# Optimization experiments

Hardware: AMD Instinct MI355X
Metric: run time of the kernel (lower is better)

Reference implementation:

```python
import jax, jax.numpy as jnp
import numpy as np

ALPHA = 0.5
SMOOTH = 1e-05
ITERS = 10


def _max_pool3x3(x):
    # 3x3 max pool, stride 1, SAME padding on NCHW tensor
    return jax.lax.reduce_window(
        x, -jnp.inf, jax.lax.max,
        window_dimensions=(1, 1, 3, 3),
        window_strides=(1, 1, 1, 1),
        padding='SAME')


def _soft_erode(x):
    return -_max_pool3x3(-x)


def _soft_dilate(x):
    return _max_pool3x3(x)


def _soft_skeletonize(img, iterations=ITERS):
    def body(skel, _):
        eroded = _soft_erode(skel)
        temp = _soft_dilate(eroded)
        skel = skel - (skel - eroded) * temp
        skel = jnp.clip(skel, 0.0, 1.0)
        return skel, None
    skel, _ = jax.lax.scan(body, img, None, length=iterations)
    return skel


def _dice_score(pred, target, smooth=SMOOTH):
    inter = jnp.sum(pred * target, axis=(2, 3))
    union = jnp.sum(pred, axis=(2, 3)) + jnp.sum(target, axis=(2, 3))
    dice = (2.0 * inter + smooth) / (union + smooth)
    return jnp.mean(dice)


def setup_inputs() -> dict:
    key = jax.random.key(0)
    k1, k2 = jax.random.split(key)
    B, C, H, W = 32, 1, 512, 512
    pred_logits = jax.random.normal(k1, (B, C, H, W), dtype=jnp.float32)
    target = jax.random.uniform(k2, (B, C, H, W), dtype=jnp.float32)
    return {"pred_logits": pred_logits, "target": target}


def reference(pred_logits, target):
    pred = jax.nn.sigmoid(pred_logits)
    dice = _dice_score(pred, target)
    pred_skel = _soft_skeletonize(pred)
    target_skel = _soft_skeletonize(target)
    skel_dice = _dice_score(pred_skel, target_skel)
    loss = (1.0 - ALPHA) * (1.0 - dice) + ALPHA * (1.0 - skel_dice)
    return (loss, dice, skel_dice)
```

## Files before the change

### kernel.cpp

```cpp
#include <hip/hip_runtime.h>
#include <hip/hip_fp16.h>
#include <math.h>


#define H 512
#define W 512
#define IMG (H * W)
#define NIMG 64
#define NPRED 32

#define APU 40
#define AROWS 74
#define BP2 38
#define BROWS 68

#define PINF2 0x7C007C00u
#define NINF2 0xFC00FC00u
#define ONE2  0x3C003C00u

typedef _Float16 f16;
typedef _Float16 h2 __attribute__((ext_vector_type(2)));
typedef __fp16 fp16v2 __attribute__((ext_vector_type(2)));

__device__ __forceinline__ uint pack2(float a, float b) {
    fp16v2 h = __builtin_amdgcn_cvt_pkrtz(a, b);
    return __builtin_bit_cast(uint, h);
}

__device__ __forceinline__ uint pmin(uint a, uint b) {
    uint d; asm("v_pk_min_f16 %0, %1, %2" : "=v"(d) : "v"(a), "v"(b)); return d;
}
__device__ __forceinline__ uint pmax(uint a, uint b) {
    uint d; asm("v_pk_max_f16 %0, %1, %2" : "=v"(d) : "v"(a), "v"(b)); return d;
}
__device__ __forceinline__ uint abit(uint hi, uint lo) {
    return __builtin_amdgcn_alignbit(hi, lo, 16);
}

__device__ __forceinline__ float wsum64(float v) {
#pragma unroll
    for (int o = 32; o > 0; o >>= 1) v += __shfl_down(v, o);
    return v;
}

__device__ __forceinline__ void hmin4p(const uint* __restrict__ p, uint m[4], uint sc[2]) {
    uint2 w0 = *(const uint2*)(p);
    uint2 w1 = *(const uint2*)(p + 2);
    uint2 w2 = *(const uint2*)(p + 4);
    sc[0] = w1.x; sc[1] = w1.y;
    uint s01 = abit(w0.y, w0.x);
    uint s12 = abit(w1.x, w0.y);
    uint s23 = abit(w1.y, w1.x);
    uint s34 = abit(w2.x, w1.y);
    uint s45 = abit(w2.y, w2.x);
    m[0] = pmin(s01, pmin(w0.y, s12));
    m[1] = pmin(s12, pmin(w1.x, s23));
    m[2] = pmin(s23, pmin(w1.y, s34));
    m[3] = pmin(s34, pmin(w2.x, s45));
}

__device__ __forceinline__ void erodep(const uint a[4], const uint b[4], const uint c[4],
                                       bool rowok, const bool eok[4], uint e[4]) {
#pragma unroll
    for (int i = 0; i < 4; i++) {
        uint v = pmin(a[i], pmin(b[i], c[i]));
        e[i] = (rowok && eok[i]) ? v : NINF2;
    }
}

__device__ __forceinline__ void hmaxp(const uint e[4], uint hx[2], uint ec[2]) {
    uint a12 = abit(e[1], e[0]);
    uint a23 = abit(e[2], e[1]);
    uint a34 = abit(e[3], e[2]);
    hx[0] = pmax(a12, pmax(e[1], a23));
    hx[1] = pmax(a23, pmax(e[2], a34));
    ec[0] = e[1]; ec[1] = e[2];
}

__device__ __forceinline__ uint upd_pair(uint s, uint ec, uint t) {
    h2 sh = __builtin_bit_cast(h2, s);
    h2 eh = __builtin_bit_cast(h2, ec);
    h2 th = __builtin_bit_cast(h2, t);
    h2 o = sh - (sh - eh) * th;
    return pmin(pmax(__builtin_bit_cast(uint, o), 0u), ONE2);
}

template<int SIG>
__device__ float2 fillA_f32p(uint* __restrict__ A, const float* __restrict__ src,
                             const float* __restrict__ tgt,
                             int tileX, int tileY, int tid) {
    float a = 0.0f, b = 0.0f;
    for (int it = tid; it < AROWS * 20; it += 256) {
        int r = it / 20;
        int u2 = it - r * 20;
        int gy = tileY + r - 4;
        int gx = tileX - 8 + 4 * u2;
        uint2 v = make_uint2(PINF2, PINF2);
        if (r < 72 && (unsigned)(u2 - 1) < 18u && (unsigned)gy < (unsigned)H &&
            (unsigned)gx < (unsigned)W) {
            float4 f = *(const float4*)(src + (size_t)gy * W + gx);
            if (SIG) {
                f.x = 1.0f / (1.0f + __expf(-f.x));
                f.y = 1.0f / (1.0f + __expf(-f.y));
                f.z = 1.0f / (1.0f + __expf(-f.z));
                f.w = 1.0f / (1.0f + __expf(-f.w));
            }
            if (((unsigned)(gx - tileX) < 64u) && ((unsigned)(gy - tileY) < 64u)) {
                if (SIG) {
                    float4 t = *(const float4*)(tgt + (size_t)gy * W + gx);
                    a += f.x * t.x + f.y * t.y + f.z * t.z + f.w * t.w;
                    b += f.x + f.y + f.z + f.w;
                } else {
                    a += f.x + f.y + f.z + f.w;
                }
            }
            v.x = pack2(f.x, f.y);
            v.y = pack2(f.z, f.w);
        }
        *(uint2*)(A + r * APU + 2 * u2) = v;
    }
    return make_float2(a, b);
}

__device__ void fillA_f16p(uint* __restrict__ A, const f16* __restrict__ src,
                           int tileX, int tileY, int tid) {
    for (int it = tid; it < AROWS * 20; it += 256) {
        int r = it / 20;
        int u2 = it - r * 20;
        int gy = tileY + r - 4;
        int gx = tileX - 8 + 4 * u2;
        uint2 v = make_uint2(PINF2, PINF2);
        if (r < 72 && (unsigned)(u2 - 1) < 18u && (unsigned)gy < (unsigned)H &&
            (unsigned)gx < (unsigned)W) {
            v = *(const uint2*)(src + (size_t)gy * W + gx);
        }
        *(uint2*)(A + r * APU + 2 * u2) = v;
    }
}

__device__ void stage1(const uint* __restrict__ Au, uint* __restrict__ Bu,
                       int tileX, int tileY, int tid) {
    for (int item = tid; item < 252; item += 256) {
        const int s = item / 18;
        const int q = item - s * 18;
        const int gcb = tileX - 4 + 4 * q;
        const int ys = tileY - 2 + 5 * s;
        bool eok[4], wok[2];
#pragma unroll
        for (int i = 0; i < 4; i++) eok[i] = ((unsigned)(gcb - 2 + 2 * i) < 511u);
        wok[0] = ((unsigned)gcb < 511u);
        wok[1] = ((unsigned)(gcb + 2) < 511u);
        const int lr = 5 * s + 2;
        const uint* Ab = Au + 2 * q;
        uint m[3][4], sc[3][2], hx[3][2], e[4], ec_cur[2], ec_nxt[2], tsc[2];
        hmin4p(Ab + (lr - 2) * APU, m[0], tsc);
        hmin4p(Ab + (lr - 1) * APU, m[1], tsc);
        hmin4p(Ab + (lr + 0) * APU, m[2], sc[0]);
        erodep(m[0], m[1], m[2], (unsigned)(ys - 1) < (unsigned)H, eok, e);
        hmaxp(e, hx[0], ec_nxt);
        hmin4p(Ab + (lr + 1) * APU, m[0], sc[1]);
        erodep(m[1], m[2], m[0], (unsigned)ys < (unsigned)H, eok, e);
        hmaxp(e, hx[1], ec_cur);
#pragma unroll
        for (int k = 0; k < 5; k++) {
            hmin4p(Ab + (lr + 2 + k) * APU, m[(k + 1) % 3], sc[(2 + k) % 3]);
            erodep(m[(k + 2) % 3], m[k % 3], m[(k + 1) % 3],
                   (unsigned)(ys + k + 1) < (unsigned)H, eok, e);
            hmaxp(e, hx[(k + 2) % 3], ec_nxt);
            int br = 5 * s + k;
            if (br < BROWS) {
                uint t0 = pmax(hx[k % 3][0], pmax(hx[(k + 1) % 3][0], hx[(k + 2) % 3][0]));
                uint t1 = pmax(hx[k % 3][1], pmax(hx[(k + 1) % 3][1], hx[(k + 2) % 3][1]));
                uint o0 = upd_pair(sc[k % 3][0], ec_cur[0], t0);
                uint o1 = upd_pair(sc[k % 3][1], ec_cur[1], t1);
                bool rin = ((unsigned)(ys + k) < (unsigned)H);
                uint2 wv;
                wv.x = (rin && wok[0]) ? o0 : PINF2;
                wv.y = (rin && wok[1]) ? o1 : PINF2;
                *(uint2*)(Bu + br * BP2 + 2 * q) = wv;
            }
            ec_cur[0] = ec_nxt[0]; ec_cur[1] = ec_nxt[1];
        }
    }
}

template<bool TOREG>
__device__ void stage2(const uint* __restrict__ Bu, int tileX, int tileY,
                       int tx, int ty, f16* __restrict__ gdst, float (*oreg)[4]) {
    const int X = tileX + 4 * tx;
    const int gy0 = tileY + 4 * ty;
    const int rb = 4 * ty + 2;
    bool eok[4];
    eok[0] = (X != 0);
    eok[1] = true;
    eok[2] = true;
    eok[3] = (X + 4 < W);
    const uint* Bb = Bu + 2 * tx;
    uint m[3][4], sc[3][2], hx[3][2], e[4], ec_cur[2], ec_nxt[2], tsc[2];
    hmin4p(Bb + (rb - 2) * BP2, m[0], tsc);
    hmin4p(Bb + (rb - 1) * BP2, m[1], tsc);
    hmin4p(Bb + (rb + 0) * BP2, m[2], sc[0]);
    erodep(m[0], m[1], m[2], (unsigned)(gy0 - 1) < (unsigned)H, eok, e);
    hmaxp(e, hx[0], ec_nxt);
    hmin4p(Bb + (rb + 1) * BP2, m[0], sc[1]);
    erodep(m[1], m[2], m[0], true, eok, e);
    hmaxp(e, hx[1], ec_cur);
#pragma unroll
    for (int k = 0; k < 4; k++) {
        hmin4p(Bb + (rb + 2 + k) * BP2, m[(k + 1) % 3], sc[(2 + k) % 3]);
        erodep(m[(k + 2) % 3], m[k % 3], m[(k + 1) % 3],
               (unsigned)(gy0 + k + 1) < (unsigned)H, eok, e);
        hmaxp(e, hx[(k + 2) % 3], ec_nxt);
        uint t0 = pmax(hx[k % 3][0], pmax(hx[(k + 1) % 3][0], hx[(k + 2) % 3][0]));
        uint t1 = pmax(hx[k % 3][1], pmax(hx[(k + 1) % 3][1], hx[(k + 2) % 3][1]));
        uint o0 = upd_pair(sc[k % 3][0], ec_cur[0], t0);
        uint o1 = upd_pair(sc[k % 3][1], ec_cur[1], t1);
        if (TOREG) {
            h2 a = __builtin_bit_cast(h2, o0);
            h2 b = __builtin_bit_cast(h2, o1);
            oreg[k][0] = (float)a.x; oreg[k][1] = (float)a.y;
            oreg[k][2] = (float)b.x; oreg[k][3] = (float)b.y;
        } else {
            *(uint2*)(gdst + (size_t)(gy0 + k) * W + X) = make_uint2(o0, o1);
        }
        ec_cur[0] = ec_nxt[0]; ec_cur[1] = ec_nxt[1];
    }
}

__global__ __launch_bounds__(256, 6) void k_first(
    const float* __restrict__ logits, const float* __restrict__ target,
    f16* __restrict__ outb, float* __restrict__ parts0, float* __restrict__ parts1) {
    __shared__ __align__(16) uint A[AROWS * APU];
    __shared__ __align__(16) uint Bu[BROWS * BP2];
    __shared__ float red[8];
    const int img = blockIdx.z;
    const int tileX = blockIdx.x * 64, tileY = blockIdx.y * 64;
    const int tid = threadIdx.y * 16 + threadIdx.x;
    const bool pred = (img < NPRED);
    float2 ab;
    if (pred) ab = fillA_f32p<1>(A, logits + (size_t)img * IMG,
                                 target + (size_t)img * IMG, tileX, tileY, tid);
    else      ab = fillA_f32p<0>(A, target + (size_t)(img - NPRED) * IMG,
                                 nullptr, tileX, tileY, tid);
    __syncthreads();
    float a = wsum64(ab.x), b = wsum64(ab.y);
    if ((tid & 63) == 0) { red[tid >> 6] = a; red[4 + (tid >> 6)] = b; }
    stage1(A, Bu, tileX, tileY, tid);
    __syncthreads();
    if (tid == 0) {
        int bi = blockIdx.z * 64 + blockIdx.y * 8 + blockIdx.x;
        parts0[bi] = red[0] + red[1] + red[2] + red[3];
        parts1[bi] = red[4] + red[5] + red[6] + red[7];
    }
    stage2<false>(Bu, tileX, tileY, threadIdx.x, threadIdx.y,
                  outb + (size_t)img * IMG, nullptr);
}

__global__ __launch_bounds__(256, 6) void k_mid(
    const f16* __restrict__ in, f16* __restrict__ outb) {
    __shared__ __align__(16) uint A[AROWS * APU];
    __shared__ __align__(16) uint Bu[BROWS * BP2];
    const int img = blockIdx.z;
    const int tileX = blockIdx.x * 64, tileY = blockIdx.y * 64;
    const int tid = threadIdx.y * 16 + threadIdx.x;
    fillA_f16p(A, in + (size_t)img * IMG, tileX, tileY, tid);
    __syncthreads();
    stage1(A, Bu, tileX, tileY, tid);
    __syncthreads();
    stage2<false>(Bu, tileX, tileY, threadIdx.x, threadIdx.y,
                  outb + (size_t)img * IMG, nullptr);
}

__global__ __launch_bounds__(256, 6) void k_last(
    const f16* __restrict__ in, float* __restrict__ pA,
    float* __restrict__ pB, float* __restrict__ pC) {
    __shared__ __align__(16) uint A[AROWS * APU];
    __shared__ __align__(16) uint Bu[BROWS * BP2];
    __shared__ float red[12];
    const int img = blockIdx.z;
    const int tileX = blockIdx.x * 64, tileY = blockIdx.y * 64;
    const int tid = threadIdx.y * 16 + threadIdx.x;
    float op[4][4], ot[4][4];
    fillA_f16p(A, in + (size_t)img * IMG, tileX, tileY, tid);
    __syncthreads();
    stage1(A, Bu, tileX, tileY, tid);
    __syncthreads();
    stage2<true>(Bu, tileX, tileY, threadIdx.x, threadIdx.y, nullptr, op);
    fillA_f16p(A, in + (size_t)(img + NPRED) * IMG, tileX, tileY, tid);
    __syncthreads();
    stage1(A, Bu, tileX, tileY, tid);
    __syncthreads();
    stage2<true>(Bu, tileX, tileY, threadIdx.x, threadIdx.y, nullptr, ot);
    float a = 0.0f, b = 0.0f, c = 0.0f;
#pragma unroll
    for (int k = 0; k < 4; k++)
#pragma unroll
        for (int j = 0; j < 4; j++) {
            a += op[k][j] * ot[k][j];
            b += op[k][j];
            c += ot[k][j];
        }
    a = wsum64(a); b = wsum64(b); c = wsum64(c);
    if ((tid & 63) == 0) {
        red[tid >> 6] = a; red[4 + (tid >> 6)] = b; red[8 + (tid >> 6)] = c;
    }
    __syncthreads();
    if (tid == 0) {
        int bi = img * 64 + blockIdx.y * 8 + blockIdx.x;
        pA[bi] = red[0] + red[1] + red[2] + red[3];
        pB[bi] = red[4] + red[5] + red[6] + red[7];
        pC[bi] = red[8] + red[9] + red[10] + red[11];
    }
}

__global__ __launch_bounds__(64) void finalize_img(
    const float* __restrict__ parts0, const float* __restrict__ parts1,
    const float* __restrict__ pA, const float* __restrict__ pB,
    const float* __restrict__ pC, float* __restrict__ dices) {
    const int i = blockIdx.x, t = threadIdx.x;
    float inter = wsum64(parts0[i * 64 + t]);
    float sp = wsum64(parts1[i * 64 + t]);
    float st = wsum64(parts0[(NPRED + i) * 64 + t]);
    float i2 = wsum64(pA[i * 64 + t]);
    float sp2 = wsum64(pB[i * 64 + t]);
    float st2 = wsum64(pC[i * 64 + t]);
    if (t == 0) {
        dices[i] = (float)((2.0 * (double)inter + 1e-5) / ((double)sp + (double)st + 1e-5));
        dices[32 + i] = (float)((2.0 * (double)i2 + 1e-5) / ((double)sp2 + (double)st2 + 1e-5));
    }
}

__global__ void finalize_out(const float* __restrict__ dices, float* __restrict__ out) {
    const int t = threadIdx.x;
    double d = 0.0, sd = 0.0;
    if (t < 32) { d = dices[t]; sd = dices[32 + t]; }
#pragma unroll
    for (int o = 32; o > 0; o >>= 1) { d += __shfl_down(d, o); sd += __shfl_down(sd, o); }
    if (t == 0) {
        d *= (1.0 / 32.0); sd *= (1.0 / 32.0);
        out[0] = (float)(0.5 * (1.0 - d) + 0.5 * (1.0 - sd));
        out[1] = (float)d;
        out[2] = (float)sd;
    }
}

extern "C" void kernel_launch(void* const* d_in, const int* in_sizes, int n_in,
                              void* d_out, int out_size, void* d_ws, size_t ws_size,
                              hipStream_t stream) {
    (void)in_sizes; (void)n_in; (void)out_size; (void)ws_size;
    const float* logits = (const float*)d_in[0];
    const float* target = (const float*)d_in[1];
    float* out = (float*)d_out;
    f16* buf0 = (f16*)d_ws;
    f16* buf1 = buf0 + (size_t)NIMG * IMG;
    float* parts0 = (float*)(buf1 + (size_t)NIMG * IMG);
    float* parts1 = parts0 + 4096;
    float* pA = parts1 + 4096;
    float* pB = pA + 2048;
    float* pC = pB + 2048;
    float* dices = pC + 2048;

    dim3 blk(16, 16, 1);
    k_first<<<dim3(8, 8, NIMG), blk, 0, stream>>>(logits, target, buf0, parts0, parts1);
    k_mid<<<dim3(8, 8, NIMG), blk, 0, stream>>>(buf0, buf1);
    k_mid<<<dim3(8, 8, NIMG), blk, 0, stream>>>(buf1, buf0);
    k_mid<<<dim3(8, 8, NIMG), blk, 0, stream>>>(buf0, buf1);
    k_last<<<dim3(8, 8, NPRED), blk, 0, stream>>>(buf1, pA, pB, pC);
    finalize_img<<<32, 64, 0, stream>>>(parts0, parts1, pA, pB, pC, dices);
    finalize_out<<<1, 64, 0, stream>>>(dices, out);
}
```

Baseline: 265.6 us.

## Widen tiles to 128x64 with 8-pixel-per-thread work and edge-specialized interior paths

Tiles grow from 64x64 to 128x64, and each thread now handles 8 fp16 pixels per row using 16-byte LDS and global accesses instead of 4. This shrinks the relative halo overhead, both in redundant loads and in recomputed halo rows and columns. Kernels are templated on an EDGE flag so interior blocks skip all boundary predicates. The trade-offs are more registers per thread (launch bounds lowered from 6 to 4 blocks), fewer blocks overall, and larger LDS tiles.

```diff
diff --git a/kernel.cpp b/kernel.cpp
--- a/kernel.cpp
+++ b/kernel.cpp
@@ -9,10 +9,13 @@
 #define NIMG 64
 #define NPRED 32
 
-#define APU 40
+#define APU 72
 #define AROWS 74
-#define BP2 38
+#define BPU 68
 #define BROWS 68
+#define TQ 17
+#define S1ITEMS 238
+#define FILLN (AROWS * 18)
 
 #define PINF2 0x7C007C00u
 #define NINF2 0xFC00FC00u
@@ -22,11 +25,14 @@
 typedef _Float16 h2 __attribute__((ext_vector_type(2)));
 typedef __fp16 fp16v2 __attribute__((ext_vector_type(2)));
 
+__device__ __forceinline__ float2 unpack2(uint u) {
+    fp16v2 h = __builtin_bit_cast(fp16v2, u);
+    return make_float2((float)h.x, (float)h.y);
+}
 __device__ __forceinline__ uint pack2(float a, float b) {
     fp16v2 h = __builtin_amdgcn_cvt_pkrtz(a, b);
     return __builtin_bit_cast(uint, h);
 }
-
 __device__ __forceinline__ uint pmin(uint a, uint b) {
     uint d; asm("v_pk_min_f16 %0, %1, %2" : "=v"(d) : "v"(a), "v"(b)); return d;
 }
@@ -43,38 +49,37 @@
     return v;
 }
 
-__device__ __forceinline__ void hmin4p(const uint* __restrict__ p, uint m[4], uint sc[2]) {
-    uint2 w0 = *(const uint2*)(p);
-    uint2 w1 = *(const uint2*)(p + 2);
-    uint2 w2 = *(const uint2*)(p + 4);
-    sc[0] = w1.x; sc[1] = w1.y;
-    uint s01 = abit(w0.y, w0.x);
-    uint s12 = abit(w1.x, w0.y);
-    uint s23 = abit(w1.y, w1.x);
-    uint s34 = abit(w2.x, w1.y);
-    uint s45 = abit(w2.y, w2.x);
-    m[0] = pmin(s01, pmin(w0.y, s12));
-    m[1] = pmin(s12, pmin(w1.x, s23));
-    m[2] = pmin(s23, pmin(w1.y, s34));
-    m[3] = pmin(s34, pmin(w2.x, s45));
-}
-
-__device__ __forceinline__ void erodep(const uint a[4], const uint b[4], const uint c[4],
-                                       bool rowok, const bool eok[4], uint e[4]) {
-#pragma unroll
-    for (int i = 0; i < 4; i++) {
+__device__ __forceinline__ void hmin8p(const uint* __restrict__ p, uint m[6], uint sc[4]) {
+    uint4 w0 = *(const uint4*)(p);
+    uint4 w1 = *(const uint4*)(p + 4);
+    uint w[8] = {w0.x, w0.y, w0.z, w0.w, w1.x, w1.y, w1.z, w1.w};
+    sc[0] = w[2]; sc[1] = w[3]; sc[2] = w[4]; sc[3] = w[5];
+    uint s[7];
+#pragma unroll
+    for (int j = 0; j < 7; j++) s[j] = abit(w[j + 1], w[j]);
+#pragma unroll
+    for (int i = 0; i < 6; i++) m[i] = pmin(s[i], pmin(w[i + 1], s[i + 1]));
+}
+
+template<bool EDGE>
+__device__ __forceinline__ void erode8(const uint a[6], const uint b[6], const uint c[6],
+                                       bool rowok, const bool* eok, uint e[6]) {
+#pragma unroll
+    for (int i = 0; i < 6; i++) {
         uint v = pmin(a[i], pmin(b[i], c[i]));
-        e[i] = (rowok && eok[i]) ? v : NINF2;
-    }
-}
-
-__device__ __forceinline__ void hmaxp(const uint e[4], uint hx[2], uint ec[2]) {
-    uint a12 = abit(e[1], e[0]);
-    uint a23 = abit(e[2], e[1]);
-    uint a34 = abit(e[3], e[2]);
-    hx[0] = pmax(a12, pmax(e[1], a23));
-    hx[1] = pmax(a23, pmax(e[2], a34));
-    ec[0] = e[1]; ec[1] = e[2];
+        e[i] = EDGE ? ((rowok && eok[i]) ? v : NINF2) : v;
+    }
+}
+
+__device__ __forceinline__ void hmax8(const uint e[6], uint hx[4], uint ec[4]) {
+    uint a[5];
+#pragma unroll
+    for (int j = 0; j < 5; j++) a[j] = abit(e[j + 1], e[j]);
+#pragma unroll
+    for (int p = 0; p < 4; p++) {
+        hx[p] = pmax(a[p], pmax(e[p + 1], a[p + 1]));
+        ec[p] = e[p + 1];
+    }
 }
 
 __device__ __forceinline__ uint upd_pair(uint s, uint ec, uint t) {
@@ -85,228 +90,284 @@
     return pmin(pmax(__builtin_bit_cast(uint, o), 0u), ONE2);
 }
 
-template<int SIG>
-__device__ float2 fillA_f32p(uint* __restrict__ A, const float* __restrict__ src,
-                             const float* __restrict__ tgt,
-                             int tileX, int tileY, int tid) {
+template<bool EDGE, int SIG>
+__device__ float2 fillA_f32(uint* __restrict__ A, const float* __restrict__ src,
+                            const float* __restrict__ tgt,
+                            int tileX, int tileY, int tid) {
     float a = 0.0f, b = 0.0f;
-    for (int it = tid; it < AROWS * 20; it += 256) {
-        int r = it / 20;
-        int u2 = it - r * 20;
-        int gy = tileY + r - 4;
-        int gx = tileX - 8 + 4 * u2;
-        uint2 v = make_uint2(PINF2, PINF2);
-        if (r < 72 && (unsigned)(u2 - 1) < 18u && (unsigned)gy < (unsigned)H &&
-            (unsigned)gx < (unsigned)W) {
-            float4 f = *(const float4*)(src + (size_t)gy * W + gx);
+    for (int i = tid; i < FILLN; i += 256) {
+        const int r = i / 18;
+        const int q = i - 18 * r;
+        const int gy = tileY + r - 4;
+        const int gx = tileX - 8 + 8 * q;
+        uint4 v = make_uint4(PINF2, PINF2, PINF2, PINF2);
+        const bool ok = EDGE ? (r < 72 && (unsigned)gy < (unsigned)H &&
+                                (unsigned)gx < (unsigned)W)
+                             : true;
+        if (ok) {
+            const float* sp = src + (size_t)gy * W + gx;
+            float4 f0 = *(const float4*)(sp);
+            float4 f1 = *(const float4*)(sp + 4);
             if (SIG) {
-                f.x = 1.0f / (1.0f + __expf(-f.x));
-                f.y = 1.0f / (1.0f + __expf(-f.y));
-                f.z = 1.0f / (1.0f + __expf(-f.z));
-                f.w = 1.0f / (1.0f + __expf(-f.w));
+                f0.x = 1.0f / (1.0f + __expf(-f0.x));
+                f0.y = 1.0f / (1.0f + __expf(-f0.y));
+                f0.z = 1.0f / (1.0f + __expf(-f0.z));
+                f0.w = 1.0f / (1.0f + __expf(-f0.w));
+                f1.x = 1.0f / (1.0f + __expf(-f1.x));
+                f1.y = 1.0f / (1.0f + __expf(-f1.y));
+                f1.z = 1.0f / (1.0f + __expf(-f1.z));
+                f1.w = 1.0f / (1.0f + __expf(-f1.w));
             }
-            if (((unsigned)(gx - tileX) < 64u) && ((unsigned)(gy - tileY) < 64u)) {
+            if (((unsigned)(r - 4) < 64u) && ((unsigned)(q - 1) < 16u)) {
                 if (SIG) {
-                    float4 t = *(const float4*)(tgt + (size_t)gy * W + gx);
-                    a += f.x * t.x + f.y * t.y + f.z * t.z + f.w * t.w;
-                    b += f.x + f.y + f.z + f.w;
+                    const float* tp = tgt + (size_t)gy * W + gx;
+                    float4 t0 = *(const float4*)(tp);
+                    float4 t1 = *(const float4*)(tp + 4);
+                    a += f0.x * t0.x + f0.y * t0.y + f0.z * t0.z + f0.w * t0.w
+                       + f1.x * t1.x + f1.y * t1.y + f1.z * t1.z + f1.w * t1.w;
+                    b += f0.x + f0.y + f0.z + f0.w + f1.x + f1.y + f1.z + f1.w;
                 } else {
-                    a += f.x + f.y + f.z + f.w;
+                    a += f0.x + f0.y + f0.z + f0.w + f1.x + f1.y + f1.z + f1.w;
                 }
             }
-            v.x = pack2(f.x, f.y);
-            v.y = pack2(f.z, f.w);
+            v.x = pack2(f0.x, f0.y); v.y = pack2(f0.z, f0.w);
+            v.z = pack2(f1.x, f1.y); v.w = pack2(f1.z, f1.w);
         }
-        *(uint2*)(A + r * APU + 2 * u2) = v;
+        *(uint4*)(A + r * APU + 4 * q) = v;
     }
     return make_float2(a, b);
 }
 
-__device__ void fillA_f16p(uint* __restrict__ A, const f16* __restrict__ src,
-                           int tileX, int tileY, int tid) {
-    for (int it = tid; it < AROWS * 20; it += 256) {
-        int r = it / 20;
-        int u2 = it - r * 20;
-        int gy = tileY + r - 4;
-        int gx = tileX - 8 + 4 * u2;
-        uint2 v = make_uint2(PINF2, PINF2);
-        if (r < 72 && (unsigned)(u2 - 1) < 18u && (unsigned)gy < (unsigned)H &&
-            (unsigned)gx < (unsigned)W) {
-            v = *(const uint2*)(src + (size_t)gy * W + gx);
+template<bool EDGE>
+__device__ void fillA_f16(uint* __restrict__ A, const f16* __restrict__ src,
+                          int tileX, int tileY, int tid) {
+    for (int i = tid; i < FILLN; i += 256) {
+        const int r = i / 18;
+        const int q = i - 18 * r;
+        const int gy = tileY + r - 4;
+        const int gx = tileX - 8 + 8 * q;
+        uint4 v;
+        if (EDGE) {
+            v = make_uint4(PINF2, PINF2, PINF2, PINF2);
+            if (r < 72 && (unsigned)gy < (unsigned)H && (unsigned)gx < (unsigned)W)
+                v = *(const uint4*)(src + (size_t)gy * W + gx);
+        } else {
+            v = *(const uint4*)(src + (size_t)gy * W + gx);
         }
-        *(uint2*)(A + r * APU + 2 * u2) = v;
-    }
-}
-
+        *(uint4*)(A + r * APU + 4 * q) = v;
+    }
+}
+
+template<bool EDGE>
 __device__ void stage1(const uint* __restrict__ Au, uint* __restrict__ Bu,
                        int tileX, int tileY, int tid) {
-    for (int item = tid; item < 252; item += 256) {
-        const int s = item / 18;
-        const int q = item - s * 18;
-        const int gcb = tileX - 4 + 4 * q;
-        const int ys = tileY - 2 + 5 * s;
-        bool eok[4], wok[2];
-#pragma unroll
-        for (int i = 0; i < 4; i++) eok[i] = ((unsigned)(gcb - 2 + 2 * i) < 511u);
-        wok[0] = ((unsigned)gcb < 511u);
-        wok[1] = ((unsigned)(gcb + 2) < 511u);
-        const int lr = 5 * s + 2;
-        const uint* Ab = Au + 2 * q;
-        uint m[3][4], sc[3][2], hx[3][2], e[4], ec_cur[2], ec_nxt[2], tsc[2];
-        hmin4p(Ab + (lr - 2) * APU, m[0], tsc);
-        hmin4p(Ab + (lr - 1) * APU, m[1], tsc);
-        hmin4p(Ab + (lr + 0) * APU, m[2], sc[0]);
-        erodep(m[0], m[1], m[2], (unsigned)(ys - 1) < (unsigned)H, eok, e);
-        hmaxp(e, hx[0], ec_nxt);
-        hmin4p(Ab + (lr + 1) * APU, m[0], sc[1]);
-        erodep(m[1], m[2], m[0], (unsigned)ys < (unsigned)H, eok, e);
-        hmaxp(e, hx[1], ec_cur);
-#pragma unroll
-        for (int k = 0; k < 5; k++) {
-            hmin4p(Ab + (lr + 2 + k) * APU, m[(k + 1) % 3], sc[(2 + k) % 3]);
-            erodep(m[(k + 2) % 3], m[k % 3], m[(k + 1) % 3],
-                   (unsigned)(ys + k + 1) < (unsigned)H, eok, e);
-            hmaxp(e, hx[(k + 2) % 3], ec_nxt);
-            int br = 5 * s + k;
-            if (br < BROWS) {
-                uint t0 = pmax(hx[k % 3][0], pmax(hx[(k + 1) % 3][0], hx[(k + 2) % 3][0]));
-                uint t1 = pmax(hx[k % 3][1], pmax(hx[(k + 1) % 3][1], hx[(k + 2) % 3][1]));
-                uint o0 = upd_pair(sc[k % 3][0], ec_cur[0], t0);
-                uint o1 = upd_pair(sc[k % 3][1], ec_cur[1], t1);
-                bool rin = ((unsigned)(ys + k) < (unsigned)H);
-                uint2 wv;
-                wv.x = (rin && wok[0]) ? o0 : PINF2;
-                wv.y = (rin && wok[1]) ? o1 : PINF2;
-                *(uint2*)(Bu + br * BP2 + 2 * q) = wv;
+    if (tid >= S1ITEMS) return;
+    const int s = tid / TQ;
+    const int g = tid - TQ * s;
+    const int gcb = tileX + 8 * g - 4;
+    const int ys = tileY - 2 + 5 * s;
+    bool eok[6], wok[4];
+    if (EDGE) {
+#pragma unroll
+        for (int i = 0; i < 6; i++) eok[i] = ((unsigned)(gcb - 2 + 2 * i) < (unsigned)W);
+#pragma unroll
+        for (int p = 0; p < 4; p++) wok[p] = ((unsigned)(gcb + 2 * p) < (unsigned)W);
+    }
+    const int lr = 5 * s + 2;
+    const uint* Ab = Au + 4 * g;
+    uint m[3][6], sc[3][4], hx[3][4], e[6], ec_cur[4], ec_nxt[4], tsc[4];
+    hmin8p(Ab + (lr - 2) * APU, m[0], tsc);
+    hmin8p(Ab + (lr - 1) * APU, m[1], tsc);
+    hmin8p(Ab + (lr + 0) * APU, m[2], sc[0]);
+    erode8<EDGE>(m[0], m[1], m[2], (unsigned)(ys - 1) < (unsigned)H, eok, e);
+    hmax8(e, hx[0], ec_nxt);
+    hmin8p(Ab + (lr + 1) * APU, m[0], sc[1]);
+    erode8<EDGE>(m[1], m[2], m[0], (unsigned)ys < (unsigned)H, eok, e);
+    hmax8(e, hx[1], ec_cur);
+#pragma unroll
+    for (int k = 0; k < 5; k++) {
+        hmin8p(Ab + (lr + 2 + k) * APU, m[(k + 1) % 3], sc[(2 + k) % 3]);
+        erode8<EDGE>(m[(k + 2) % 3], m[k % 3], m[(k + 1) % 3],
+                     (unsigned)(ys + k + 1) < (unsigned)H, eok, e);
+        hmax8(e, hx[(k + 2) % 3], ec_nxt);
+        const int br = 5 * s + k;
+        if (br < BROWS) {
+            const bool rin = EDGE ? ((unsigned)(ys + k) < (unsigned)H) : true;
+            uint o[4];
+#pragma unroll
+            for (int p = 0; p < 4; p++) {
+                uint t = pmax(hx[k % 3][p], pmax(hx[(k + 1) % 3][p], hx[(k + 2) % 3][p]));
+                uint v = upd_pair(sc[k % 3][p], ec_cur[p], t);
+                o[p] = EDGE ? ((rin && wok[p]) ? v : PINF2) : v;
             }
-            ec_cur[0] = ec_nxt[0]; ec_cur[1] = ec_nxt[1];
+            *(uint4*)(Bu + br * BPU + 4 * g) = make_uint4(o[0], o[1], o[2], o[3]);
         }
-    }
-}
-
-template<bool TOREG>
-__device__ void stage2(const uint* __restrict__ Bu, int tileX, int tileY,
-                       int tx, int ty, f16* __restrict__ gdst, float (*oreg)[4]) {
-    const int X = tileX + 4 * tx;
+#pragma unroll
+        for (int p = 0; p < 4; p++) ec_cur[p] = ec_nxt[p];
+    }
+}
+
+template<bool EDGE, bool TOREG>
+__device__ void stage2(const uint* __restrict__ Bu, int tileX, int tileY, int tid,
+                       f16* __restrict__ gdst, uint* __restrict__ oreg) {
+    const int g = tid & 15;
+    const int ty = tid >> 4;
+    const int X = tileX + 8 * g;
     const int gy0 = tileY + 4 * ty;
     const int rb = 4 * ty + 2;
-    bool eok[4];
-    eok[0] = (X != 0);
-    eok[1] = true;
-    eok[2] = true;
-    eok[3] = (X + 4 < W);
-    const uint* Bb = Bu + 2 * tx;
-    uint m[3][4], sc[3][2], hx[3][2], e[4], ec_cur[2], ec_nxt[2], tsc[2];
-    hmin4p(Bb + (rb - 2) * BP2, m[0], tsc);
-    hmin4p(Bb + (rb - 1) * BP2, m[1], tsc);
-    hmin4p(Bb + (rb + 0) * BP2, m[2], sc[0]);
-    erodep(m[0], m[1], m[2], (unsigned)(gy0 - 1) < (unsigned)H, eok, e);
-    hmaxp(e, hx[0], ec_nxt);
-    hmin4p(Bb + (rb + 1) * BP2, m[0], sc[1]);
-    erodep(m[1], m[2], m[0], true, eok, e);
-    hmaxp(e, hx[1], ec_cur);
+    bool eok[6];
+    if (EDGE) {
+#pragma unroll
+        for (int i = 0; i < 6; i++) eok[i] = ((unsigned)(X - 2 + 2 * i) < (unsigned)W);
+    }
+    const uint* Bb = Bu + 4 * g;
+    uint m[3][6], sc[3][4], hx[3][4], e[6], ec_cur[4], ec_nxt[4], tsc[4];
+    hmin8p(Bb + (rb - 2) * BPU, m[0], tsc);
+    hmin8p(Bb + (rb - 1) * BPU, m[1], tsc);
+    hmin8p(Bb + (rb + 0) * BPU, m[2], sc[0]);
+    erode8<EDGE>(m[0], m[1], m[2], (unsigned)(gy0 - 1) < (unsigned)H, eok, e);
+    hmax8(e, hx[0], ec_nxt);
+    hmin8p(Bb + (rb + 1) * BPU, m[0], sc[1]);
+    erode8<EDGE>(m[1], m[2], m[0], true, eok, e);
+    hmax8(e, hx[1], ec_cur);
 #pragma unroll
     for (int k = 0; k < 4; k++) {
-        hmin4p(Bb + (rb + 2 + k) * BP2, m[(k + 1) % 3], sc[(2 + k) % 3]);
-        erodep(m[(k + 2) % 3], m[k % 3], m[(k + 1) % 3],
-               (unsigned)(gy0 + k + 1) < (unsigned)H, eok, e);
-        hmaxp(e, hx[(k + 2) % 3], ec_nxt);
-        uint t0 = pmax(hx[k % 3][0], pmax(hx[(k + 1) % 3][0], hx[(k + 2) % 3][0]));
-        uint t1 = pmax(hx[k % 3][1], pmax(hx[(k + 1) % 3][1], hx[(k + 2) % 3][1]));
-        uint o0 = upd_pair(sc[k % 3][0], ec_cur[0], t0);
-        uint o1 = upd_pair(sc[k % 3][1], ec_cur[1], t1);
+        hmin8p(Bb + (rb + 2 + k) * BPU, m[(k + 1) % 3], sc[(2 + k) % 3]);
+        erode8<EDGE>(m[(k + 2) % 3], m[k % 3], m[(k + 1) % 3],
+                     (unsigned)(gy0 + k + 1) < (unsigned)H, eok, e);
+        hmax8(e, hx[(k + 2) % 3], ec_nxt);
+        uint o[4];
+#pragma unroll
+        for (int p = 0; p < 4; p++) {
+            uint t = pmax(hx[k % 3][p], pmax(hx[(k + 1) % 3][p], hx[(k + 2) % 3][p]));
+            o[p] = upd_pair(sc[k % 3][p], ec_cur[p], t);
+        }
         if (TOREG) {
-            h2 a = __builtin_bit_cast(h2, o0);
-            h2 b = __builtin_bit_cast(h2, o1);
-            oreg[k][0] = (float)a.x; oreg[k][1] = (float)a.y;
-            oreg[k][2] = (float)b.x; oreg[k][3] = (float)b.y;
+#pragma unroll
+            for (int p = 0; p < 4; p++) oreg[4 * k + p] = o[p];
         } else {
-            *(uint2*)(gdst + (size_t)(gy0 + k) * W + X) = make_uint2(o0, o1);
+            *(uint4*)(gdst + (size_t)(gy0 + k) * W + X) = make_uint4(o[0], o[1], o[2], o[3]);
         }
-        ec_cur[0] = ec_nxt[0]; ec_cur[1] = ec_nxt[1];
-    }
-}
-
-__global__ __launch_bounds__(256, 6) void k_first(
+#pragma unroll
+        for (int p = 0; p < 4; p++) ec_cur[p] = ec_nxt[p];
+    }
+}
+
+__device__ __forceinline__ bool is_edge() {
+    return (blockIdx.x == 0) | (blockIdx.x == 3) | (blockIdx.y == 0) | (blockIdx.y == 7);
+}
+
+__global__ __launch_bounds__(256, 4) void k_first(
     const float* __restrict__ logits, const float* __restrict__ target,
     f16* __restrict__ outb, float* __restrict__ parts0, float* __restrict__ parts1) {
     __shared__ __align__(16) uint A[AROWS * APU];
-    __shared__ __align__(16) uint Bu[BROWS * BP2];
+    __shared__ __align__(16) uint Bu[BROWS * BPU];
     __shared__ float red[8];
     const int img = blockIdx.z;
-    const int tileX = blockIdx.x * 64, tileY = blockIdx.y * 64;
-    const int tid = threadIdx.y * 16 + threadIdx.x;
+    const int tileX = blockIdx.x * 128, tileY = blockIdx.y * 64;
+    const int tid = threadIdx.x;
     const bool pred = (img < NPRED);
+    const bool edge = is_edge();
     float2 ab;
-    if (pred) ab = fillA_f32p<1>(A, logits + (size_t)img * IMG,
-                                 target + (size_t)img * IMG, tileX, tileY, tid);
-    else      ab = fillA_f32p<0>(A, target + (size_t)(img - NPRED) * IMG,
-                                 nullptr, tileX, tileY, tid);
+    if (edge) {
+        if (pred) ab = fillA_f32<true, 1>(A, logits + (size_t)img * IMG,
+                                          target + (size_t)img * IMG, tileX, tileY, tid);
+        else      ab = fillA_f32<true, 0>(A, target + (size_t)(img - NPRED) * IMG,
+                                          nullptr, tileX, tileY, tid);
+    } else {
+        if (pred) ab = fillA_f32<false, 1>(A, logits + (size_t)img * IMG,
+                                           target + (size_t)img * IMG, tileX, tileY, tid);
+        else      ab = fillA_f32<false, 0>(A, target + (size_t)(img - NPRED) * IMG,
+                                           nullptr, tileX, tileY, tid);
+    }
     __syncthreads();
     float a = wsum64(ab.x), b = wsum64(ab.y);
     if ((tid & 63) == 0) { red[tid >> 6] = a; red[4 + (tid >> 6)] = b; }
-    stage1(A, Bu, tileX, tileY, tid);
+    if (edge) stage1<true>(A, Bu, tileX, tileY, tid);
+    else      stage1<false>(A, Bu, tileX, tileY, tid);
     __syncthreads();
     if (tid == 0) {
-        int bi = blockIdx.z * 64 + blockIdx.y * 8 + blockIdx.x;
+        int bi = blockIdx.z * 32 + blockIdx.y * 4 + blockIdx.x;
         parts0[bi] = red[0] + red[1] + red[2] + red[3];
         parts1[bi] = red[4] + red[5] + red[6] + red[7];
     }
-    stage2<false>(Bu, tileX, tileY, threadIdx.x, threadIdx.y,
-                  outb + (size_t)img * IMG, nullptr);
-}
-
-__global__ __launch_bounds__(256, 6) void k_mid(
+    if (edge) stage2<true, false>(Bu, tileX, tileY, tid, outb + (size_t)img * IMG, nullptr);
+    else      stage2<false, false>(Bu, tileX, tileY, tid, outb + (size_t)img * IMG, nullptr);
+}
+
+__global__ __launch_bounds__(256, 4) void k_mid(
     const f16* __restrict__ in, f16* __restrict__ outb) {
     __shared__ __align__(16) uint A[AROWS * APU];
-    __shared__ __align__(16) uint Bu[BROWS * BP2];
+    __shared__ __align__(16) uint Bu[BROWS * BPU];
     const int img = blockIdx.z;
-    const int tileX = blockIdx.x * 64, tileY = blockIdx.y * 64;
-    const int tid = threadIdx.y * 16 + threadIdx.x;
-    fillA_f16p(A, in + (size_t)img * IMG, tileX, tileY, tid);
-    __syncthreads();
-    stage1(A, Bu, tileX, tileY, tid);
-    __syncthreads();
-    stage2<false>(Bu, tileX, tileY, threadIdx.x, threadIdx.y,
-                  outb + (size_t)img * IMG, nullptr);
-}
-
-__global__ __launch_bounds__(256, 6) void k_last(
+    const int tileX = blockIdx.x * 128, tileY = blockIdx.y * 64;
+    const int tid = threadIdx.x;
+    const bool edge = is_edge();
+    if (edge) {
+        fillA_f16<true>(A, in + (size_t)img * IMG, tileX, tileY, tid);
+        __syncthreads();
+        stage1<true>(A, Bu, tileX, tileY, tid);
+        __syncthreads();
+        stage2<true, false>(Bu, tileX, tileY, tid, outb + (size_t)img * IMG, nullptr);
+    } else {
+        fillA_f16<false>(A, in + (size_t)img * IMG, tileX, tileY, tid);
+        __syncthreads();
+        stage1<false>(A, Bu, tileX, tileY, tid);
+        __syncthreads();
+        stage2<false, false>(Bu, tileX, tileY, tid, outb + (size_t)img * IMG, nullptr);
+    }
+}
+
+__global__ __launch_bounds__(256, 4) void k_last(
     const f16* __restrict__ in, float* __restrict__ pA,
     float* __restrict__ pB, float* __restrict__ pC) {
     __shared__ __align__(16) uint A[AROWS * APU];
-    __shared__ __align__(16) uint Bu[BROWS * BP2];
+    __shared__ __align__(16) uint Bu[BROWS * BPU];
     __shared__ float red[12];
     const int img = blockIdx.z;
-    const int tileX = blockIdx.x * 64, tileY = blockIdx.y * 64;
-    const int tid = threadIdx.y * 16 + threadIdx.x;
-    float op[4][4], ot[4][4];
-    fillA_f16p(A, in + (size_t)img * IMG, tileX, tileY, tid);
-    __syncthreads();
-    stage1(A, Bu, tileX, tileY, tid);
-    __syncthreads();
-    stage2<true>(Bu, tileX, tileY, threadIdx.x, threadIdx.y, nullptr, op);
-    fillA_f16p(A, in + (size_t)(img + NPRED) * IMG, tileX, tileY, tid);
-    __syncthreads();
-    stage1(A, Bu, tileX, tileY, tid);
-    __syncthreads();
-    stage2<true>(Bu, tileX, tileY, threadIdx.x, threadIdx.y, nullptr, ot);
+    const int tileX = blockIdx.x * 128, tileY = blockIdx.y * 64;
+    const int tid = threadIdx.x;
+    const bool edge = is_edge();
+    uint op[16], ot[16];
+    if (edge) {
+        fillA_f16<true>(A, in + (size_t)img * IMG, tileX, tileY, tid);
+        __syncthreads();
+        stage1<true>(A, Bu, tileX, tileY, tid);
+        __syncthreads();
+        stage2<true, true>(Bu, tileX, tileY, tid, nullptr, op);
+        fillA_f16<true>(A, in + (size_t)(img + NPRED) * IMG, tileX, tileY, tid);
+        __syncthreads();
+        stage1<true>(A, Bu, tileX, tileY, tid);
+        __syncthreads();
+        stage2<true, true>(Bu, tileX, tileY, tid, nullptr, ot);
+    } else {
+        fillA_f16<false>(A, in + (size_t)img * IMG, tileX, tileY, tid);
+        __syncthreads();
+        stage1<false>(A, Bu, tileX, tileY, tid);
+        __syncthreads();
+        stage2<false, true>(Bu, tileX, tileY, tid, nullptr, op);
+        fillA_f16<false>(A, in + (size_t)(img + NPRED) * IMG, tileX, tileY, tid);
+        __syncthreads();
+        stage1<false>(A, Bu, tileX, tileY, tid);
+        __syncthreads();
+        stage2<false, true>(Bu, tileX, tileY, tid, nullptr, ot);
+    }
     float a = 0.0f, b = 0.0f, c = 0.0f;
 #pragma unroll
-    for (int k = 0; k < 4; k++)
-#pragma unroll
-        for (int j = 0; j < 4; j++) {
-            a += op[k][j] * ot[k][j];
-            b += op[k][j];
-            c += ot[k][j];
-        }
+    for (int j = 0; j < 16; j++) {
+        float2 p = unpack2(op[j]);
+        float2 t = unpack2(ot[j]);
+        a += p.x * t.x + p.y * t.y;
+        b += p.x + p.y;
+        c += t.x + t.y;
+    }
     a = wsum64(a); b = wsum64(b); c = wsum64(c);
     if ((tid & 63) == 0) {
         red[tid >> 6] = a; red[4 + (tid >> 6)] = b; red[8 + (tid >> 6)] = c;
     }
     __syncthreads();
     if (tid == 0) {
-        int bi = img * 64 + blockIdx.y * 8 + blockIdx.x;
+        int bi = img * 32 + blockIdx.y * 4 + blockIdx.x;
         pA[bi] = red[0] + red[1] + red[2] + red[3];
         pB[bi] = red[4] + red[5] + red[6] + red[7];
         pC[bi] = red[8] + red[9] + red[10] + red[11];
@@ -318,12 +379,13 @@
     const float* __restrict__ pA, const float* __restrict__ pB,
     const float* __restrict__ pC, float* __restrict__ dices) {
     const int i = blockIdx.x, t = threadIdx.x;
-    float inter = wsum64(parts0[i * 64 + t]);
-    float sp = wsum64(parts1[i * 64 + t]);
-    float st = wsum64(parts0[(NPRED + i) * 64 + t]);
-    float i2 = wsum64(pA[i * 64 + t]);
-    float sp2 = wsum64(pB[i * 64 + t]);
-    float st2 = wsum64(pC[i * 64 + t]);
+    const bool v = (t < 32);
+    float inter = wsum64(v ? parts0[i * 32 + t] : 0.0f);
+    float sp = wsum64(v ? parts1[i * 32 + t] : 0.0f);
+    float st = wsum64(v ? parts0[(NPRED + i) * 32 + t] : 0.0f);
+    float i2 = wsum64(v ? pA[i * 32 + t] : 0.0f);
+    float sp2 = wsum64(v ? pB[i * 32 + t] : 0.0f);
+    float st2 = wsum64(v ? pC[i * 32 + t] : 0.0f);
     if (t == 0) {
         dices[i] = (float)((2.0 * (double)inter + 1e-5) / ((double)sp + (double)st + 1e-5));
         dices[32 + i] = (float)((2.0 * (double)i2 + 1e-5) / ((double)sp2 + (double)st2 + 1e-5));
@@ -354,18 +416,18 @@
     f16* buf0 = (f16*)d_ws;
     f16* buf1 = buf0 + (size_t)NIMG * IMG;
     float* parts0 = (float*)(buf1 + (size_t)NIMG * IMG);
-    float* parts1 = parts0 + 4096;
-    float* pA = parts1 + 4096;
-    float* pB = pA + 2048;
-    float* pC = pB + 2048;
-    float* dices = pC + 2048;
-
-    dim3 blk(16, 16, 1);
-    k_first<<<dim3(8, 8, NIMG), blk, 0, stream>>>(logits, target, buf0, parts0, parts1);
-    k_mid<<<dim3(8, 8, NIMG), blk, 0, stream>>>(buf0, buf1);
-    k_mid<<<dim3(8, 8, NIMG), blk, 0, stream>>>(buf1, buf0);
-    k_mid<<<dim3(8, 8, NIMG), blk, 0, stream>>>(buf0, buf1);
-    k_last<<<dim3(8, 8, NPRED), blk, 0, stream>>>(buf1, pA, pB, pC);
+    float* parts1 = parts0 + 2048;
+    float* pA = parts1 + 2048;
+    float* pB = pA + 1024;
+    float* pC = pB + 1024;
+    float* dices = pC + 1024;
+
+    dim3 blk(256, 1, 1);
+    k_first<<<dim3(4, 8, NIMG), blk, 0, stream>>>(logits, target, buf0, parts0, parts1);
+    k_mid<<<dim3(4, 8, NIMG), blk, 0, stream>>>(buf0, buf1);
+    k_mid<<<dim3(4, 8, NIMG), blk, 0, stream>>>(buf1, buf0);
+    k_mid<<<dim3(4, 8, NIMG), blk, 0, stream>>>(buf0, buf1);
+    k_last<<<dim3(4, 8, NPRED), blk, 0, stream>>>(buf1, pA, pB, pC);
     finalize_img<<<32, 64, 0, stream>>>(parts0, parts1, pA, pB, pC, dices);
     finalize_out<<<1, 64, 0, stream>>>(dices, out);
 }
```

New measurement: 227.6 us. 14.3% less time.
